# Kernel tuning notes

Hardware: AMD Instinct MI355X
Metric: run time of the kernel (lower is better)

Reference implementation:

```python
import jax, jax.numpy as jnp
import numpy as np

HEAD_DIM = 128
MAX_TIMESCALE = 10000.0
MIN_TIMESCALE = 1.0


def _rope(x, pos):
    # x: [B, S, H, D], pos: [B, S]
    d = x.shape[-1]
    fraction = 2.0 * jnp.arange(0, d // 2, dtype=jnp.float32) / d
    timescale = MIN_TIMESCALE * (MAX_TIMESCALE / MIN_TIMESCALE) ** fraction  # [D/2]
    sinusoid = pos.astype(jnp.float32)[..., None, None] / timescale  # [B,S,1,D/2]
    sin, cos = jnp.sin(sinusoid), jnp.cos(sinusoid)
    xf = x.astype(jnp.float32)
    x1, x2 = jnp.split(xf, 2, axis=-1)
    return jnp.concatenate((x1 * cos - x2 * sin, x2 * cos + x1 * sin), axis=-1).astype(x.dtype)


def setup_inputs() -> dict:
    key = jax.random.key(0)
    ks = jax.random.split(key, 5)
    B, T, D, N, K, H = 2, 2048, 2048, 16, 4, HEAD_DIM
    s = 0.02
    X = jax.random.normal(ks[0], (B, T, D), dtype=jnp.float32)
    q_positions = jnp.broadcast_to(jnp.arange(T, dtype=jnp.int32), (B, T))
    Wq = jax.random.normal(ks[1], (D, N, H), dtype=jnp.float32) * s
    Wk = jax.random.normal(ks[2], (D, K, H), dtype=jnp.float32) * s
    Wv = jax.random.normal(ks[3], (D, K, H), dtype=jnp.float32) * s
    Wo = jax.random.normal(ks[4], (N, H, D), dtype=jnp.float32) * s
    return {"X": X, "q_positions": q_positions, "Wq": Wq, "Wk": Wk, "Wv": Wv, "Wo": Wo}


def reference(X, q_positions, Wq, Wk, Wv, Wo):
    B, T, D = X.shape
    N, K = Wq.shape[1], Wk.shape[1]
    groups = N // K
    # fused QKV projections (DenseGeneral, no bias)
    q = jnp.einsum('btd,dnh->btnh', X, Wq)  # [B,T,N,H]
    k = jnp.einsum('btd,dkh->btkh', X, Wk)  # [B,T,K,H]
    v = jnp.einsum('btd,dkh->btkh', X, Wv)  # [B,T,K,H]
    # RoPE (note: original uses q_positions sin/cos for both q and k in the no-cache path)
    q = _rope(q, q_positions)
    k = _rope(k, q_positions)
    # GQA: broadcast kv heads to query heads
    k = jnp.repeat(k, groups, axis=2)  # [B,T,N,H]
    v = jnp.repeat(v, groups, axis=2)
    # attention with scale=1.0 and causal masking
    scores = jnp.einsum('btnh,bsnh->bnts', q, k)  # [B,N,T,T]
    causal = jnp.tril(jnp.ones((T, T), dtype=bool))
    scores = jnp.where(causal, scores, jnp.finfo(scores.dtype).min)
    probs = jax.nn.softmax(scores, axis=-1)
    attn = jnp.einsum('bnts,bsnh->btnh', probs, v)  # [B,T,N,H]
    # output projection contracting (head, head_dim)
    out = jnp.einsum('btnh,nhd->btd', attn, Wo)
    return out.astype(X.dtype)
```

## Files before the change

kernel.cpp:

```cpp
#include <hip/hip_runtime.h>
#include <math.h>

#define DEVI static __device__ __forceinline__

using f16x8 = __attribute__((ext_vector_type(8))) _Float16;
using h16x2 = __attribute__((ext_vector_type(2))) __fp16;
using f32x4  = __attribute__((ext_vector_type(4))) float;
using f32x16 = __attribute__((ext_vector_type(16))) float;

constexpr int Bb = 2, Tt = 2048, Dd = 2048, NQ = 16, NK = 4, HD = 128;
constexpr int Mrows = Bb * Tt;
constexpr int QKVC  = NQ*HD + 2*NK*HD;
constexpr int KOFF  = NQ*HD;
constexpr int VOFF  = NQ*HD + NK*HD;

DEVI ushort f2h(float f) {
  _Float16 h = (_Float16)f;
  union { _Float16 h; ushort u; } v; v.h = h;
  return v.u;
}
DEVI float h2f(ushort u) {
  union { ushort u; _Float16 h; } v; v.u = u;
  return (float)v.h;
}

typedef const __attribute__((address_space(1))) unsigned* gp1;
typedef __attribute__((address_space(3))) unsigned* lp3;
DEVI void gload16(void* lds, const void* g) {
  __builtin_amdgcn_global_load_lds((gp1)g, (lp3)lds, 16, 0, 0);
}

__global__ void k_cvt(const float* __restrict__ x, ushort* __restrict__ o, int n4) {
  int i = blockIdx.x * blockDim.x + threadIdx.x;
  if (i >= n4) return;
  float4 v = ((const float4*)x)[i];
  ushort4 u;
  u.x = f2h(v.x); u.y = f2h(v.y); u.z = f2h(v.z); u.w = f2h(v.w);
  ((ushort4*)o)[i] = u;
}

__global__ void k_tconv(const float* __restrict__ in, ushort* __restrict__ out, int R, int C) {
  __shared__ float t[32][33];
  const int c0 = blockIdx.x * 32, r0 = blockIdx.y * 32;
  const int tx = threadIdx.x, ty = threadIdx.y;
#pragma unroll
  for (int i = 0; i < 32; i += 8)
    t[ty + i][tx] = in[(size_t)(r0 + ty + i) * C + (c0 + tx)];
  __syncthreads();
#pragma unroll
  for (int i = 0; i < 32; i += 8)
    out[(size_t)(c0 + ty + i) * R + (r0 + tx)] = f2h(t[tx][ty + i]);
}

DEVI void stv(float* p, float v)  { *p = v; }
DEVI void stv(ushort* p, float v) { *p = f2h(v); }

template <typename OT>
__launch_bounds__(256)
__global__ void k_gemm_bt(const ushort* __restrict__ A, const ushort* __restrict__ Bt,
                          OT* __restrict__ C, int M, int N, int Kd) {
  __shared__ char As[8192];
  __shared__ char Bs[8192];
  const int tid = threadIdx.x;
  const int l = tid & 63, w = tid >> 6;
  const int wr = w >> 1, wc = w & 1;
  const int lr = l & 15, lk = l >> 4;
  const size_t row0 = (size_t)blockIdx.y * 128, col0 = (size_t)blockIdx.x * 128;

  f32x4 acc[4][4];
#pragma unroll
  for (int i = 0; i < 4; ++i)
#pragma unroll
    for (int j = 0; j < 4; ++j) acc[i][j] = (f32x4){0.f, 0.f, 0.f, 0.f};

  const int c0i = tid, c1i = tid + 256;
  const int ra0 = c0i >> 2, sa0 = (c0i & 3) ^ ((ra0 >> 1) & 3);
  const int ra1 = c1i >> 2, sa1 = (c1i & 3) ^ ((ra1 >> 1) & 3);

  for (int kt = 0; kt < Kd; kt += 32) {
    if (kt) __syncthreads();
    gload16(As + c0i * 16, A + (row0 + ra0) * Kd + kt + sa0 * 8);
    gload16(As + c1i * 16, A + (row0 + ra1) * Kd + kt + sa1 * 8);
    gload16(Bs + c0i * 16, Bt + (col0 + ra0) * Kd + kt + sa0 * 8);
    gload16(Bs + c1i * 16, Bt + (col0 + ra1) * Kd + kt + sa1 * 8);
    __syncthreads();
    f16x8 af[4], bfr[4];
#pragma unroll
    for (int i = 0; i < 4; ++i) {
      int ra = wr * 64 + i * 16 + lr;
      af[i] = *(const f16x8*)(As + ra * 64 + ((lk ^ ((ra >> 1) & 3)) << 4));
      int rb = wc * 64 + i * 16 + lr;
      bfr[i] = *(const f16x8*)(Bs + rb * 64 + ((lk ^ ((rb >> 1) & 3)) << 4));
    }
#pragma unroll
    for (int i = 0; i < 4; ++i)
#pragma unroll
      for (int j = 0; j < 4; ++j)
        acc[i][j] = __builtin_amdgcn_mfma_f32_16x16x32_f16(af[i], bfr[j], acc[i][j], 0, 0, 0);
  }
#pragma unroll
  for (int i = 0; i < 4; ++i) {
    size_t r = row0 + wr * 64 + i * 16 + lk * 4;
#pragma unroll
    for (int j = 0; j < 4; ++j) {
      size_t cc = col0 + wc * 64 + j * 16 + lr;
#pragma unroll
      for (int rg = 0; rg < 4; ++rg) stv(&C[(r + rg) * N + cc], acc[i][j][rg]);
    }
  }
}

__global__ void k_rope_tab(const int* __restrict__ pos, float* __restrict__ tab) {
  int idx = blockIdx.x * blockDim.x + threadIdx.x;
  if (idx >= Mrows * 64) return;
  int m = idx >> 6, i = idx & 63;
  double a = (double)pos[m] * exp2(-0.20762050593045952 * (double)i);
  tab[idx * 2]     = (float)cos(a);
  tab[idx * 2 + 1] = (float)sin(a);
}

__global__ void k_rope(ushort* __restrict__ qkv, const float* __restrict__ tab) {
  int idx = blockIdx.x * blockDim.x + threadIdx.x;
  if (idx >= Mrows * 20 * 8) return;
  int chunk = idx & 7;
  int h20 = (idx >> 3) % 20;
  int m = idx / 160;
  int colbase = (h20 < 16) ? h20 * 128 : (KOFF + (h20 - 16) * 128);
  size_t base = (size_t)m * QKVC + colbase + chunk * 8;
  union { uint4 v; ushort s[8]; } A1, A2, O1, O2;
  A1.v = *(const uint4*)(qkv + base);
  A2.v = *(const uint4*)(qkv + base + 64);
  const float* tp = tab + ((size_t)m * 64 + chunk * 8) * 2;
#pragma unroll
  for (int j = 0; j < 8; ++j) {
    float c = tp[2 * j], s = tp[2 * j + 1];
    float x1 = h2f(A1.s[j]), x2 = h2f(A2.s[j]);
    O1.s[j] = f2h(x1 * c - x2 * s);
    O2.s[j] = f2h(x2 * c + x1 * s);
  }
  *(uint4*)(qkv + base) = O1.v;
  *(uint4*)(qkv + base + 64) = O2.v;
}

__global__ void k_vt(const ushort* __restrict__ qkv, ushort* __restrict__ vt) {
  __shared__ ushort t[32][33];
  const int bg = blockIdx.z, bq = bg >> 2, g = bg & 3;
  const int s0 = blockIdx.x * 32, h0 = blockIdx.y * 32;
  const int tx = threadIdx.x, ty = threadIdx.y;
#pragma unroll
  for (int i = 0; i < 32; i += 8)
    t[ty + i][tx] = qkv[(size_t)(bq * Tt + s0 + ty + i) * QKVC + VOFF + g * HD + h0 + tx];
  __syncthreads();
  const int sx = (tx & 3) | ((tx & 8) >> 1) | ((tx & 4) << 1) | (tx & 16);
#pragma unroll
  for (int i = 0; i < 32; i += 8)
    vt[((size_t)bg * HD + h0 + ty + i) * Tt + (s0 + sx)] = t[tx][ty + i];
}

__launch_bounds__(256, 2)
__global__ void k_flash(const ushort* __restrict__ qkv, const ushort* __restrict__ vt,
                        ushort* __restrict__ attn) {
  __shared__ char Ks[2][16384];
  __shared__ char Vs[2][16384];
  const int b = blockIdx.x;
  const int vv = b >> 8, u = b & 255;
  const int hid = u >> 3, p = u & 7;
  const int qt = vv ? p : (15 - p);
  const int bq = hid >> 4, n = hid & 15, g = n >> 2;
  const int tid = threadIdx.x, w = tid >> 6, l = tid & 63;
  const int q5 = l & 31, hi = l >> 5;
  const int t0 = qt * 128;
  const int qrow = t0 + w * 32;
  const int qglob = qrow + q5;

  f16x8 qf[8];
  {
    const size_t qb = ((size_t)(bq * Tt + qglob)) * QKVC + n * HD + hi * 8;
#pragma unroll
    for (int kc = 0; kc < 8; ++kc) qf[kc] = *(const f16x8*)(qkv + qb + kc * 16);
  }
  f32x16 O[4];
#pragma unroll
  for (int ht = 0; ht < 4; ++ht)
#pragma unroll
    for (int r = 0; r < 16; ++r) O[ht][r] = 0.f;
  float m = -INFINITY, lsum = 0.f;

  const size_t kgbase = (size_t)(bq * Tt) * QKVC + KOFF + g * HD;
  const size_t vgbase = (size_t)(bq * 4 + g) * HD * Tt;
  const int ntiles = 2 * qt + 2;

#define STAGE(buf, s0s)                                                               \
  {                                                                                   \
    _Pragma("unroll")                                                                 \
    for (int cc = 0; cc < 4; ++cc) {                                                  \
      int c = cc * 256 + tid;                                                         \
      int sK = c >> 4, gK = (c & 15) ^ (sK & 15);                                     \
      gload16(Ks[buf] + c * 16, qkv + kgbase + (size_t)((s0s) + sK) * QKVC + gK * 8); \
      int hV = c >> 3, gV = (c & 7) ^ (hV & 7);                                       \
      gload16(Vs[buf] + c * 16, vt + vgbase + (size_t)hV * Tt + (s0s) + gV * 8);      \
    }                                                                                 \
  }

  STAGE(0, 0);
  __syncthreads();

  for (int j = 0; j < ntiles; ++j) {
    const int cur = j & 1;
    if (j + 1 < ntiles) STAGE(cur ^ 1, (j + 1) * 64);
    const int s0 = j * 64;
    if (s0 <= qrow + 31) {
      f32x16 sc[2];
      __builtin_amdgcn_s_setprio(1);
#pragma unroll
      for (int st = 0; st < 2; ++st) {
        f32x16 a;
#pragma unroll
        for (int r = 0; r < 16; ++r) a[r] = 0.f;
        const int sl = st * 32 + q5;
        const int ssw = (sl & 15) << 4;
#pragma unroll
        for (int kc = 0; kc < 8; ++kc) {
          f16x8 kf = *(const f16x8*)(Ks[cur] + sl * 256 + (((kc * 32 + hi * 16)) ^ ssw));
          a = __builtin_amdgcn_mfma_f32_32x32x16_f16(kf, qf[kc], a, 0, 0, 0);
        }
        sc[st] = a;
      }
      __builtin_amdgcn_s_setprio(0);
      if (s0 + 63 > qrow) {
#pragma unroll
        for (int st = 0; st < 2; ++st)
#pragma unroll
          for (int r = 0; r < 16; ++r) {
            int sg = s0 + st * 32 + (r & 3) + 8 * (r >> 2) + 4 * hi;
            if (sg > qglob) sc[st][r] = -INFINITY;
          }
      }
      float pm = -INFINITY;
#pragma unroll
      for (int st = 0; st < 2; ++st)
#pragma unroll
        for (int r = 0; r < 16; ++r) pm = fmaxf(pm, sc[st][r]);
      pm = fmaxf(pm, __shfl_xor(pm, 32));
      const bool doresc = !__all(pm - m <= 8.0f);
      float scl = 1.f;
      if (doresc) { float mn = fmaxf(m, pm); scl = __expf(m - mn); m = mn; }
      float rs = 0.f;
#pragma unroll
      for (int st = 0; st < 2; ++st)
#pragma unroll
        for (int r = 0; r < 16; ++r) { sc[st][r] = __expf(sc[st][r] - m); rs += sc[st][r]; }
      rs += __shfl_xor(rs, 32);
      if (doresc) {
        float sr[16];
#pragma unroll
        for (int r = 0; r < 16; ++r) sr[r] = __shfl(scl, (r & 3) + 8 * (r >> 2) + 4 * hi);
#pragma unroll
        for (int ht = 0; ht < 4; ++ht)
#pragma unroll
          for (int r = 0; r < 16; ++r) O[ht][r] *= sr[r];
        lsum = lsum * scl + rs;
      } else {
        lsum += rs;
      }
      unsigned pw[2][8];
#pragma unroll
      for (int st = 0; st < 2; ++st)
#pragma unroll
        for (int i = 0; i < 8; ++i) {
          union { h16x2 h; unsigned u; } t;
          t.h = __builtin_amdgcn_cvt_pkrtz(sc[st][2 * i], sc[st][2 * i + 1]);
          pw[st][i] = t.u;
        }
      __builtin_amdgcn_s_setprio(1);
#pragma unroll
      for (int ht = 0; ht < 4; ++ht) {
        const int hrow = ht * 32 + q5;
        const int hsw = (hrow & 7) << 4;
#pragma unroll
        for (int cc = 0; cc < 4; ++cc) {
          const int st = cc >> 1, ch = cc & 1;
          union { unsigned u[4]; f16x8 v; } pa;
          pa.u[0] = pw[st][ch * 4 + 0];
          pa.u[1] = pw[st][ch * 4 + 1];
          pa.u[2] = pw[st][ch * 4 + 2];
          pa.u[3] = pw[st][ch * 4 + 3];
          f16x8 vf = *(const f16x8*)(Vs[cur] + hrow * 128 + (((cc * 2 + hi) << 4) ^ hsw));
          O[ht] = __builtin_amdgcn_mfma_f32_32x32x16_f16(pa.v, vf, O[ht], 0, 0, 0);
        }
      }
      __builtin_amdgcn_s_setprio(0);
    }
    __syncthreads();
  }
#undef STAGE
  float iv[16];
#pragma unroll
  for (int r = 0; r < 16; ++r) iv[r] = 1.f / __shfl(lsum, (r & 3) + 8 * (r >> 2) + 4 * hi);
#pragma unroll
  for (int ht = 0; ht < 4; ++ht)
#pragma unroll
    for (int r = 0; r < 16; ++r) {
      size_t orow = (size_t)(bq * Tt + qrow + (r & 3) + 8 * (r >> 2) + 4 * hi);
      attn[orow * 2048 + n * HD + ht * 32 + q5] = f2h(O[ht][r] * iv[r]);
    }
}

extern "C" void kernel_launch(void* const* d_in, const int* in_sizes, int n_in,
                              void* d_out, int out_size, void* d_ws, size_t ws_size,
                              hipStream_t stream) {
  const float* X  = (const float*)d_in[0];
  const int*   qp = (const int*)d_in[1];
  const float* Wq = (const float*)d_in[2];
  const float* Wk = (const float*)d_in[3];
  const float* Wv = (const float*)d_in[4];
  const float* Wo = (const float*)d_in[5];
  float* out = (float*)d_out;
  char* ws = (char*)d_ws;

  ushort* Xf    = (ushort*)(ws + 0);
  ushort* WqkvT = (ushort*)(ws + 16777216);
  ushort* WoT   = (ushort*)(ws + 29360128);
  ushort* QKV   = (ushort*)(ws + 37748736);
  ushort* VT    = (ushort*)(ws + 62914560);
  ushort* attn  = (ushort*)(ws + 67108864);
  float*  tab   = (float*)(ws + 83886080);

  dim3 tb(32, 8);
  k_cvt<<<(Mrows * Dd / 4 + 255) / 256, 256, 0, stream>>>(X, Xf, Mrows * Dd / 4);
  k_tconv<<<dim3(64, 64), tb, 0, stream>>>(Wq, WqkvT, Dd, NQ * HD);
  k_tconv<<<dim3(16, 64), tb, 0, stream>>>(Wk, WqkvT + (size_t)KOFF * Dd, Dd, NK * HD);
  k_tconv<<<dim3(16, 64), tb, 0, stream>>>(Wv, WqkvT + (size_t)VOFF * Dd, Dd, NK * HD);
  k_tconv<<<dim3(64, 64), tb, 0, stream>>>(Wo, WoT, NQ * HD, Dd);
  k_gemm_bt<ushort><<<dim3(QKVC / 128, Mrows / 128), 256, 0, stream>>>(
      Xf, WqkvT, QKV, Mrows, QKVC, Dd);
  k_rope_tab<<<(Mrows * 64 + 255) / 256, 256, 0, stream>>>(qp, tab);
  k_rope<<<(Mrows * 160 + 255) / 256, 256, 0, stream>>>(QKV, tab);
  k_vt<<<dim3(Tt / 32, HD / 32, Bb * NK), tb, 0, stream>>>(QKV, VT);
  k_flash<<<dim3(512), 256, 0, stream>>>(QKV, VT, attn);
  k_gemm_bt<float><<<dim3(Dd / 128, Mrows / 128), 256, 0, stream>>>(
      attn, WoT, out, Mrows, Dd, Dd);
}
```

Baseline: 219.0 us.

## Software-pipeline PV MFMA of previous tile behind current softmax with triple-buffered V

Restructures the flash-attention loop so the P·V matrix multiply for tile j-1 is issued after the max/rescale factor for tile j is known but before its exponentials. That lets MFMA work overlap the exp/convert VALU work. V staging moves to a three-slot LDS ring so the previous tile's V stays resident while the next is loaded, with extra drain steps after the loop. The per-tile cross-half row-sum shuffle is also deferred to a single reduction at the end. The cost is more LDS per block (80KB), which may pressure occupancy, plus more complex control flow around the causal boundary.

Result: no change. 219.3 us (+0.1%).

```diff
diff --git a/kernel.cpp b/kernel.cpp
--- a/kernel.cpp
+++ b/kernel.cpp
@@ -161,13 +161,13 @@
 __global__ void k_flash(const ushort* __restrict__ qkv, const ushort* __restrict__ vt,
                         ushort* __restrict__ attn) {
   __shared__ char Ks[2][16384];
-  __shared__ char Vs[2][16384];
+  __shared__ char Vs[3][16384];
   const int b = blockIdx.x;
   const int vv = b >> 8, u = b & 255;
   const int hid = u >> 3, p = u & 7;
   const int qt = vv ? p : (15 - p);
   const int bq = hid >> 4, n = hid & 15, g = n >> 2;
-  const int tid = threadIdx.x, w = tid >> 6, l = tid & 63;
+  const int tid = threadIdx.x, l = tid & 63, w = tid >> 6;
   const int q5 = l & 31, hi = l >> 5;
   const int t0 = qt * 128;
   const int qrow = t0 + w * 32;
@@ -185,31 +185,54 @@
 #pragma unroll
     for (int r = 0; r < 16; ++r) O[ht][r] = 0.f;
   float m = -INFINITY, lsum = 0.f;
+  unsigned pw[2][8];
 
   const size_t kgbase = (size_t)(bq * Tt) * QKVC + KOFF + g * HD;
   const size_t vgbase = (size_t)(bq * 4 + g) * HD * Tt;
   const int ntiles = 2 * qt + 2;
-
-#define STAGE(buf, s0s)                                                               \
-  {                                                                                   \
-    _Pragma("unroll")                                                                 \
-    for (int cc = 0; cc < 4; ++cc) {                                                  \
-      int c = cc * 256 + tid;                                                         \
-      int sK = c >> 4, gK = (c & 15) ^ (sK & 15);                                     \
-      gload16(Ks[buf] + c * 16, qkv + kgbase + (size_t)((s0s) + sK) * QKVC + gK * 8); \
-      int hV = c >> 3, gV = (c & 7) ^ (hV & 7);                                       \
-      gload16(Vs[buf] + c * 16, vt + vgbase + (size_t)hV * Tt + (s0s) + gV * 8);      \
-    }                                                                                 \
-  }
-
-  STAGE(0, 0);
+  const int myjmax = (qrow + 31) >> 6;
+
+#define STAGE(kb, vslot, s0s)                                                          \
+  {                                                                                    \
+    _Pragma("unroll")                                                                  \
+    for (int cc = 0; cc < 4; ++cc) {                                                   \
+      int c = cc * 256 + tid;                                                          \
+      int sK = c >> 4, gK = (c & 15) ^ (sK & 15);                                      \
+      gload16(Ks[kb] + c * 16, qkv + kgbase + (size_t)((s0s) + sK) * QKVC + gK * 8);   \
+      int hV = c >> 3, gV = (c & 7) ^ (hV & 7);                                        \
+      gload16(Vs[vslot] + c * 16, vt + vgbase + (size_t)hV * Tt + (s0s) + gV * 8);     \
+    }                                                                                  \
+  }
+
+#define PVSTEP(vbase)                                                                  \
+  {                                                                                    \
+    __builtin_amdgcn_s_setprio(1);                                                     \
+    _Pragma("unroll")                                                                  \
+    for (int ht = 0; ht < 4; ++ht) {                                                   \
+      const int hrow = ht * 32 + q5;                                                   \
+      const int hsw = (hrow & 7) << 4;                                                 \
+      _Pragma("unroll")                                                                \
+      for (int cc = 0; cc < 4; ++cc) {                                                 \
+        union { unsigned uu[4]; f16x8 v; } pa;                                         \
+        pa.uu[0] = pw[cc >> 1][(cc & 1) * 4 + 0];                                      \
+        pa.uu[1] = pw[cc >> 1][(cc & 1) * 4 + 1];                                      \
+        pa.uu[2] = pw[cc >> 1][(cc & 1) * 4 + 2];                                      \
+        pa.uu[3] = pw[cc >> 1][(cc & 1) * 4 + 3];                                      \
+        f16x8 vf = *(const f16x8*)((vbase) + hrow * 128 + (((cc * 2 + hi) << 4) ^ hsw)); \
+        O[ht] = __builtin_amdgcn_mfma_f32_32x32x16_f16(pa.v, vf, O[ht], 0, 0, 0);      \
+      }                                                                                \
+    }                                                                                  \
+    __builtin_amdgcn_s_setprio(0);                                                     \
+  }
+
+  STAGE(0, 0, 0);
   __syncthreads();
 
   for (int j = 0; j < ntiles; ++j) {
-    const int cur = j & 1;
-    if (j + 1 < ntiles) STAGE(cur ^ 1, (j + 1) * 64);
+    const int kcur = j & 1;
+    if (j + 1 < ntiles) STAGE(kcur ^ 1, (j + 1) % 3, (j + 1) * 64);
     const int s0 = j * 64;
-    if (s0 <= qrow + 31) {
+    if (j <= myjmax) {
       f32x16 sc[2];
       __builtin_amdgcn_s_setprio(1);
 #pragma unroll
@@ -221,7 +244,7 @@
         const int ssw = (sl & 15) << 4;
 #pragma unroll
         for (int kc = 0; kc < 8; ++kc) {
-          f16x8 kf = *(const f16x8*)(Ks[cur] + sl * 256 + (((kc * 32 + hi * 16)) ^ ssw));
+          f16x8 kf = *(const f16x8*)(Ks[kcur] + sl * 256 + (((kc * 32 + hi * 16)) ^ ssw));
           a = __builtin_amdgcn_mfma_f32_32x32x16_f16(kf, qf[kc], a, 0, 0, 0);
         }
         sc[st] = a;
@@ -245,12 +268,12 @@
       const bool doresc = !__all(pm - m <= 8.0f);
       float scl = 1.f;
       if (doresc) { float mn = fmaxf(m, pm); scl = __expf(m - mn); m = mn; }
+      if (j > 0) PVSTEP(Vs[(j + 2) % 3]);
       float rs = 0.f;
 #pragma unroll
       for (int st = 0; st < 2; ++st)
 #pragma unroll
         for (int r = 0; r < 16; ++r) { sc[st][r] = __expf(sc[st][r] - m); rs += sc[st][r]; }
-      rs += __shfl_xor(rs, 32);
       if (doresc) {
         float sr[16];
 #pragma unroll
@@ -263,7 +286,6 @@
       } else {
         lsum += rs;
       }
-      unsigned pw[2][8];
 #pragma unroll
       for (int st = 0; st < 2; ++st)
 #pragma unroll
@@ -272,31 +294,18 @@
           t.h = __builtin_amdgcn_cvt_pkrtz(sc[st][2 * i], sc[st][2 * i + 1]);
           pw[st][i] = t.u;
         }
-      __builtin_amdgcn_s_setprio(1);
-#pragma unroll
-      for (int ht = 0; ht < 4; ++ht) {
-        const int hrow = ht * 32 + q5;
-        const int hsw = (hrow & 7) << 4;
-#pragma unroll
-        for (int cc = 0; cc < 4; ++cc) {
-          const int st = cc >> 1, ch = cc & 1;
-          union { unsigned u[4]; f16x8 v; } pa;
-          pa.u[0] = pw[st][ch * 4 + 0];
-          pa.u[1] = pw[st][ch * 4 + 1];
-          pa.u[2] = pw[st][ch * 4 + 2];
-          pa.u[3] = pw[st][ch * 4 + 3];
-          f16x8 vf = *(const f16x8*)(Vs[cur] + hrow * 128 + (((cc * 2 + hi) << 4) ^ hsw));
-          O[ht] = __builtin_amdgcn_mfma_f32_32x32x16_f16(pa.v, vf, O[ht], 0, 0, 0);
-        }
-      }
-      __builtin_amdgcn_s_setprio(0);
+    } else if (j == myjmax + 1) {
+      PVSTEP(Vs[(j + 2) % 3]);
     }
     __syncthreads();
   }
+  if (myjmax == ntiles - 1) PVSTEP(Vs[myjmax % 3]);
 #undef STAGE
+#undef PVSTEP
+  const float ltot = lsum + __shfl_xor(lsum, 32);
   float iv[16];
 #pragma unroll
-  for (int r = 0; r < 16; ++r) iv[r] = 1.f / __shfl(lsum, (r & 3) + 8 * (r >> 2) + 4 * hi);
+  for (int r = 0; r < 16; ++r) iv[r] = 1.f / __shfl(ltot, (r & 3) + 8 * (r >> 2) + 4 * hi);
 #pragma unroll
   for (int ht = 0; ht < 4; ++ht)
 #pragma unroll
```

## Restructure flash attention to 128-key tiles with split K/V staging and exp2 softmax

Applied to the files above, without the earlier changes.

The flash kernel now processes 128-key tiles with single-buffered K and V in LDS. The next K tile loads while softmax runs and the next V tile loads after PV, with explicit waitcnt and barriers replacing the double-buffered per-64-key scheme. Q is pre-scaled by log2(e) in the RoPE kernel so softmax can use exp2f. The rescale threshold becomes 11 in log2 units, and the lsum cross-half shuffle is deferred to the end. These changes aim to cut loop overhead, barriers and per-tile shuffles. The risks are less overlap from single buffering and exposure of load latency.

Measured after the change: 296.2 us. 35.2% more time.

```diff
diff --git a/kernel.cpp b/kernel.cpp
--- a/kernel.cpp
+++ b/kernel.cpp
@@ -125,6 +125,7 @@
   int chunk = idx & 7;
   int h20 = (idx >> 3) % 20;
   int m = idx / 160;
+  const float qs = (h20 < 16) ? 1.4426950408889634f : 1.0f;
   int colbase = (h20 < 16) ? h20 * 128 : (KOFF + (h20 - 16) * 128);
   size_t base = (size_t)m * QKVC + colbase + chunk * 8;
   union { uint4 v; ushort s[8]; } A1, A2, O1, O2;
@@ -135,8 +136,8 @@
   for (int j = 0; j < 8; ++j) {
     float c = tp[2 * j], s = tp[2 * j + 1];
     float x1 = h2f(A1.s[j]), x2 = h2f(A2.s[j]);
-    O1.s[j] = f2h(x1 * c - x2 * s);
-    O2.s[j] = f2h(x2 * c + x1 * s);
+    O1.s[j] = f2h((x1 * c - x2 * s) * qs);
+    O2.s[j] = f2h((x2 * c + x1 * s) * qs);
   }
   *(uint4*)(qkv + base) = O1.v;
   *(uint4*)(qkv + base + 64) = O2.v;
@@ -160,17 +161,16 @@
 __launch_bounds__(256, 2)
 __global__ void k_flash(const ushort* __restrict__ qkv, const ushort* __restrict__ vt,
                         ushort* __restrict__ attn) {
-  __shared__ char Ks[2][16384];
-  __shared__ char Vs[2][16384];
+  __shared__ char Ks[32768];
+  __shared__ char Vs[32768];
   const int b = blockIdx.x;
   const int vv = b >> 8, u = b & 255;
   const int hid = u >> 3, p = u & 7;
   const int qt = vv ? p : (15 - p);
   const int bq = hid >> 4, n = hid & 15, g = n >> 2;
-  const int tid = threadIdx.x, w = tid >> 6, l = tid & 63;
+  const int tid = threadIdx.x, l = tid & 63, w = tid >> 6;
   const int q5 = l & 31, hi = l >> 5;
-  const int t0 = qt * 128;
-  const int qrow = t0 + w * 32;
+  const int qrow = qt * 128 + w * 32;
   const int qglob = qrow + q5;
 
   f16x8 qf[8];
@@ -188,115 +188,129 @@
 
   const size_t kgbase = (size_t)(bq * Tt) * QKVC + KOFF + g * HD;
   const size_t vgbase = (size_t)(bq * 4 + g) * HD * Tt;
-  const int ntiles = 2 * qt + 2;
-
-#define STAGE(buf, s0s)                                                               \
+  const int ntiles = qt + 1;
+
+#define STAGE_K(s0s)                                                                  \
   {                                                                                   \
     _Pragma("unroll")                                                                 \
-    for (int cc = 0; cc < 4; ++cc) {                                                  \
+    for (int cc = 0; cc < 8; ++cc) {                                                  \
       int c = cc * 256 + tid;                                                         \
       int sK = c >> 4, gK = (c & 15) ^ (sK & 15);                                     \
-      gload16(Ks[buf] + c * 16, qkv + kgbase + (size_t)((s0s) + sK) * QKVC + gK * 8); \
-      int hV = c >> 3, gV = (c & 7) ^ (hV & 7);                                       \
-      gload16(Vs[buf] + c * 16, vt + vgbase + (size_t)hV * Tt + (s0s) + gV * 8);      \
+      gload16(Ks + c * 16, qkv + kgbase + (size_t)((s0s) + sK) * QKVC + gK * 8);      \
     }                                                                                 \
   }
-
-  STAGE(0, 0);
+#define STAGE_V(s0s)                                                                  \
+  {                                                                                   \
+    _Pragma("unroll")                                                                 \
+    for (int cc = 0; cc < 8; ++cc) {                                                  \
+      int c = cc * 256 + tid;                                                         \
+      int hV = c >> 4, gV = (c & 15) ^ (hV & 15);                                     \
+      gload16(Vs + c * 16, vt + vgbase + (size_t)hV * Tt + (s0s) + gV * 8);           \
+    }                                                                                 \
+  }
+
+  STAGE_K(0);
+  STAGE_V(0);
   __syncthreads();
 
   for (int j = 0; j < ntiles; ++j) {
-    const int cur = j & 1;
-    if (j + 1 < ntiles) STAGE(cur ^ 1, (j + 1) * 64);
-    const int s0 = j * 64;
-    if (s0 <= qrow + 31) {
-      f32x16 sc[2];
-      __builtin_amdgcn_s_setprio(1);
-#pragma unroll
-      for (int st = 0; st < 2; ++st) {
-        f32x16 a;
-#pragma unroll
-        for (int r = 0; r < 16; ++r) a[r] = 0.f;
-        const int sl = st * 32 + q5;
-        const int ssw = (sl & 15) << 4;
-#pragma unroll
-        for (int kc = 0; kc < 8; ++kc) {
-          f16x8 kf = *(const f16x8*)(Ks[cur] + sl * 256 + (((kc * 32 + hi * 16)) ^ ssw));
-          a = __builtin_amdgcn_mfma_f32_32x32x16_f16(kf, qf[kc], a, 0, 0, 0);
+    const int s0 = j * 128;
+    f32x16 sc[4];
+    __builtin_amdgcn_s_setprio(1);
+#pragma unroll
+    for (int st = 0; st < 4; ++st) {
+      f32x16 a;
+#pragma unroll
+      for (int r = 0; r < 16; ++r) a[r] = 0.f;
+      const int sl = st * 32 + q5;
+      const int ssw = (sl & 15) << 4;
+#pragma unroll
+      for (int kc = 0; kc < 8; ++kc) {
+        f16x8 kf = *(const f16x8*)(Ks + sl * 256 + ((kc * 32 + hi * 16) ^ ssw));
+        a = __builtin_amdgcn_mfma_f32_32x32x16_f16(kf, qf[kc], a, 0, 0, 0);
+      }
+      sc[st] = a;
+    }
+    __builtin_amdgcn_s_setprio(0);
+    __syncthreads();
+    if (j + 1 < ntiles) STAGE_K(s0 + 128);
+    if (j == ntiles - 1) {
+#pragma unroll
+      for (int st = 0; st < 4; ++st)
+#pragma unroll
+        for (int r = 0; r < 16; ++r) {
+          int sg = s0 + st * 32 + (r & 3) + 8 * (r >> 2) + 4 * hi;
+          if (sg > qglob) sc[st][r] = -INFINITY;
         }
-        sc[st] = a;
+    }
+    float pm = -INFINITY;
+#pragma unroll
+    for (int st = 0; st < 4; ++st)
+#pragma unroll
+      for (int r = 0; r < 16; ++r) pm = fmaxf(pm, sc[st][r]);
+    pm = fmaxf(pm, __shfl_xor(pm, 32));
+    const bool doresc = !__all(pm - m <= 11.0f);
+    float scl = 1.f;
+    if (doresc) { float mn = fmaxf(m, pm); scl = exp2f(m - mn); m = mn; }
+    float rs = 0.f;
+#pragma unroll
+    for (int st = 0; st < 4; ++st)
+#pragma unroll
+      for (int r = 0; r < 16; ++r) { sc[st][r] = exp2f(sc[st][r] - m); rs += sc[st][r]; }
+    if (doresc) {
+      float sr[16];
+#pragma unroll
+      for (int r = 0; r < 16; ++r) sr[r] = __shfl(scl, (r & 3) + 8 * (r >> 2) + 4 * hi);
+#pragma unroll
+      for (int ht = 0; ht < 4; ++ht)
+#pragma unroll
+        for (int r = 0; r < 16; ++r) O[ht][r] *= sr[r];
+      lsum = lsum * scl + rs;
+    } else {
+      lsum += rs;
+    }
+    unsigned pw[4][8];
+#pragma unroll
+    for (int st = 0; st < 4; ++st)
+#pragma unroll
+      for (int i = 0; i < 8; ++i) {
+        union { h16x2 h; unsigned u; } t;
+        t.h = __builtin_amdgcn_cvt_pkrtz(sc[st][2 * i], sc[st][2 * i + 1]);
+        pw[st][i] = t.u;
       }
-      __builtin_amdgcn_s_setprio(0);
-      if (s0 + 63 > qrow) {
-#pragma unroll
-        for (int st = 0; st < 2; ++st)
-#pragma unroll
-          for (int r = 0; r < 16; ++r) {
-            int sg = s0 + st * 32 + (r & 3) + 8 * (r >> 2) + 4 * hi;
-            if (sg > qglob) sc[st][r] = -INFINITY;
-          }
-      }
-      float pm = -INFINITY;
-#pragma unroll
-      for (int st = 0; st < 2; ++st)
-#pragma unroll
-        for (int r = 0; r < 16; ++r) pm = fmaxf(pm, sc[st][r]);
-      pm = fmaxf(pm, __shfl_xor(pm, 32));
-      const bool doresc = !__all(pm - m <= 8.0f);
-      float scl = 1.f;
-      if (doresc) { float mn = fmaxf(m, pm); scl = __expf(m - mn); m = mn; }
-      float rs = 0.f;
-#pragma unroll
-      for (int st = 0; st < 2; ++st)
-#pragma unroll
-        for (int r = 0; r < 16; ++r) { sc[st][r] = __expf(sc[st][r] - m); rs += sc[st][r]; }
-      rs += __shfl_xor(rs, 32);
-      if (doresc) {
-        float sr[16];
-#pragma unroll
-        for (int r = 0; r < 16; ++r) sr[r] = __shfl(scl, (r & 3) + 8 * (r >> 2) + 4 * hi);
-#pragma unroll
-        for (int ht = 0; ht < 4; ++ht)
-#pragma unroll
-          for (int r = 0; r < 16; ++r) O[ht][r] *= sr[r];
-        lsum = lsum * scl + rs;
-      } else {
-        lsum += rs;
-      }
-      unsigned pw[2][8];
-#pragma unroll
-      for (int st = 0; st < 2; ++st)
-#pragma unroll
-        for (int i = 0; i < 8; ++i) {
-          union { h16x2 h; unsigned u; } t;
-          t.h = __builtin_amdgcn_cvt_pkrtz(sc[st][2 * i], sc[st][2 * i + 1]);
-          pw[st][i] = t.u;
-        }
-      __builtin_amdgcn_s_setprio(1);
-#pragma unroll
-      for (int ht = 0; ht < 4; ++ht) {
-        const int hrow = ht * 32 + q5;
-        const int hsw = (hrow & 7) << 4;
-#pragma unroll
-        for (int cc = 0; cc < 4; ++cc) {
-          const int st = cc >> 1, ch = cc & 1;
-          union { unsigned u[4]; f16x8 v; } pa;
-          pa.u[0] = pw[st][ch * 4 + 0];
-          pa.u[1] = pw[st][ch * 4 + 1];
-          pa.u[2] = pw[st][ch * 4 + 2];
-          pa.u[3] = pw[st][ch * 4 + 3];
-          f16x8 vf = *(const f16x8*)(Vs[cur] + hrow * 128 + (((cc * 2 + hi) << 4) ^ hsw));
+    __builtin_amdgcn_s_setprio(1);
+#pragma unroll
+    for (int ht = 0; ht < 4; ++ht) {
+      const int hrow = ht * 32 + q5;
+      const int hsw = (hrow & 15) << 4;
+#pragma unroll
+      for (int st = 0; st < 4; ++st)
+#pragma unroll
+        for (int ch = 0; ch < 2; ++ch) {
+          union { unsigned uu[4]; f16x8 v; } pa;
+          pa.uu[0] = pw[st][ch * 4 + 0];
+          pa.uu[1] = pw[st][ch * 4 + 1];
+          pa.uu[2] = pw[st][ch * 4 + 2];
+          pa.uu[3] = pw[st][ch * 4 + 3];
+          f16x8 vf = *(const f16x8*)(Vs + hrow * 256 + ((st * 64 + ch * 32 + hi * 16) ^ hsw));
           O[ht] = __builtin_amdgcn_mfma_f32_32x32x16_f16(pa.v, vf, O[ht], 0, 0, 0);
         }
-      }
-      __builtin_amdgcn_s_setprio(0);
-    }
-    __syncthreads();
-  }
-#undef STAGE
+    }
+    __builtin_amdgcn_s_setprio(0);
+    __builtin_amdgcn_s_barrier();
+    if (j + 1 < ntiles) {
+      STAGE_V(s0 + 128);
+      asm volatile("s_waitcnt vmcnt(8)" ::: "memory");
+    }
+    __builtin_amdgcn_s_barrier();
+    __builtin_amdgcn_sched_barrier(0);
+  }
+#undef STAGE_K
+#undef STAGE_V
+  const float ltot = lsum + __shfl_xor(lsum, 32);
   float iv[16];
 #pragma unroll
-  for (int r = 0; r < 16; ++r) iv[r] = 1.f / __shfl(lsum, (r & 3) + 8 * (r >> 2) + 4 * hi);
+  for (int r = 0; r < 16; ++r) iv[r] = 1.f / __shfl(ltot, (r & 3) + 8 * (r >> 2) + 4 * hi);
 #pragma unroll
   for (int ht = 0; ht < 4; ++ht)
 #pragma unroll
```

## Split long causal query tiles across two blocks and merge partials; use exp2 softmax

Applied to the files above, without the earlier changes.

The eight largest query tiles per head are each split into two KV ranges handled by separate blocks, which write normalized partial outputs plus (max, sum) to workspace. A new merge kernel combines the two halves, and the smaller tiles run unsplit. The aim is better load balance across the 768 blocks, at the cost of an extra launch and extra global traffic. Q is also pre-scaled by log2(e) in the RoPE kernel so softmax can use exp2f, and the lazy-rescale threshold is raised, which shifts how partial sums are kept in fp16.

Result: slower. 240.4 us (+9.7%).

```diff
diff --git a/kernel.cpp b/kernel.cpp
--- a/kernel.cpp
+++ b/kernel.cpp
@@ -125,6 +125,7 @@
   int chunk = idx & 7;
   int h20 = (idx >> 3) % 20;
   int m = idx / 160;
+  const float qs = (h20 < 16) ? 1.4426950408889634f : 1.0f;
   int colbase = (h20 < 16) ? h20 * 128 : (KOFF + (h20 - 16) * 128);
   size_t base = (size_t)m * QKVC + colbase + chunk * 8;
   union { uint4 v; ushort s[8]; } A1, A2, O1, O2;
@@ -135,8 +136,8 @@
   for (int j = 0; j < 8; ++j) {
     float c = tp[2 * j], s = tp[2 * j + 1];
     float x1 = h2f(A1.s[j]), x2 = h2f(A2.s[j]);
-    O1.s[j] = f2h(x1 * c - x2 * s);
-    O2.s[j] = f2h(x2 * c + x1 * s);
+    O1.s[j] = f2h((x1 * c - x2 * s) * qs);
+    O2.s[j] = f2h((x2 * c + x1 * s) * qs);
   }
   *(uint4*)(qkv + base) = O1.v;
   *(uint4*)(qkv + base + 64) = O2.v;
@@ -159,18 +160,33 @@
 
 __launch_bounds__(256, 2)
 __global__ void k_flash(const ushort* __restrict__ qkv, const ushort* __restrict__ vt,
-                        ushort* __restrict__ attn) {
+                        ushort* __restrict__ attn, ushort* __restrict__ pOn,
+                        float2* __restrict__ pml) {
   __shared__ char Ks[2][16384];
   __shared__ char Vs[2][16384];
   const int b = blockIdx.x;
-  const int vv = b >> 8, u = b & 255;
-  const int hid = u >> 3, p = u & 7;
-  const int qt = vv ? p : (15 - p);
+  int qt, hid, j0, j1, sp = 0, half = 0;
+  bool split;
+  if (b < 512) {
+    split = true;
+    half = b & 1;
+    sp = b >> 1;
+    qt = 15 - (b >> 6);
+    hid = sp & 31;
+    j0 = half ? (qt + 1) : 0;
+    j1 = half ? (2 * qt + 2) : (qt + 1);
+  } else {
+    split = false;
+    int c = b - 512;
+    qt = 7 - (c >> 5);
+    hid = c & 31;
+    j0 = 0;
+    j1 = 2 * qt + 2;
+  }
   const int bq = hid >> 4, n = hid & 15, g = n >> 2;
-  const int tid = threadIdx.x, w = tid >> 6, l = tid & 63;
+  const int tid = threadIdx.x, l = tid & 63, w = tid >> 6;
   const int q5 = l & 31, hi = l >> 5;
-  const int t0 = qt * 128;
-  const int qrow = t0 + w * 32;
+  const int qrow = qt * 128 + w * 32;
   const int qglob = qrow + q5;
 
   f16x8 qf[8];
@@ -188,7 +204,6 @@
 
   const size_t kgbase = (size_t)(bq * Tt) * QKVC + KOFF + g * HD;
   const size_t vgbase = (size_t)(bq * 4 + g) * HD * Tt;
-  const int ntiles = 2 * qt + 2;
 
 #define STAGE(buf, s0s)                                                               \
   {                                                                                   \
@@ -202,12 +217,12 @@
     }                                                                                 \
   }
 
-  STAGE(0, 0);
+  STAGE(0, j0 * 64);
   __syncthreads();
 
-  for (int j = 0; j < ntiles; ++j) {
-    const int cur = j & 1;
-    if (j + 1 < ntiles) STAGE(cur ^ 1, (j + 1) * 64);
+  for (int j = j0; j < j1; ++j) {
+    const int cur = (j - j0) & 1;
+    if (j + 1 < j1) STAGE(cur ^ 1, (j + 1) * 64);
     const int s0 = j * 64;
     if (s0 <= qrow + 31) {
       f32x16 sc[2];
@@ -242,15 +257,14 @@
 #pragma unroll
         for (int r = 0; r < 16; ++r) pm = fmaxf(pm, sc[st][r]);
       pm = fmaxf(pm, __shfl_xor(pm, 32));
-      const bool doresc = !__all(pm - m <= 8.0f);
+      const bool doresc = !__all(pm - m <= 11.0f);
       float scl = 1.f;
-      if (doresc) { float mn = fmaxf(m, pm); scl = __expf(m - mn); m = mn; }
+      if (doresc) { float mn = fmaxf(m, pm); scl = exp2f(m - mn); m = mn; }
       float rs = 0.f;
 #pragma unroll
       for (int st = 0; st < 2; ++st)
 #pragma unroll
-        for (int r = 0; r < 16; ++r) { sc[st][r] = __expf(sc[st][r] - m); rs += sc[st][r]; }
-      rs += __shfl_xor(rs, 32);
+        for (int r = 0; r < 16; ++r) { sc[st][r] = exp2f(sc[st][r] - m); rs += sc[st][r]; }
       if (doresc) {
         float sr[16];
 #pragma unroll
@@ -279,12 +293,11 @@
         const int hsw = (hrow & 7) << 4;
 #pragma unroll
         for (int cc = 0; cc < 4; ++cc) {
-          const int st = cc >> 1, ch = cc & 1;
-          union { unsigned u[4]; f16x8 v; } pa;
-          pa.u[0] = pw[st][ch * 4 + 0];
-          pa.u[1] = pw[st][ch * 4 + 1];
-          pa.u[2] = pw[st][ch * 4 + 2];
-          pa.u[3] = pw[st][ch * 4 + 3];
+          union { unsigned uu[4]; f16x8 v; } pa;
+          pa.uu[0] = pw[cc >> 1][(cc & 1) * 4 + 0];
+          pa.uu[1] = pw[cc >> 1][(cc & 1) * 4 + 1];
+          pa.uu[2] = pw[cc >> 1][(cc & 1) * 4 + 2];
+          pa.uu[3] = pw[cc >> 1][(cc & 1) * 4 + 3];
           f16x8 vf = *(const f16x8*)(Vs[cur] + hrow * 128 + (((cc * 2 + hi) << 4) ^ hsw));
           O[ht] = __builtin_amdgcn_mfma_f32_32x32x16_f16(pa.v, vf, O[ht], 0, 0, 0);
         }
@@ -294,16 +307,60 @@
     __syncthreads();
   }
 #undef STAGE
+  const float ltot = lsum + __shfl_xor(lsum, 32);
   float iv[16];
 #pragma unroll
-  for (int r = 0; r < 16; ++r) iv[r] = 1.f / __shfl(lsum, (r & 3) + 8 * (r >> 2) + 4 * hi);
-#pragma unroll
-  for (int ht = 0; ht < 4; ++ht)
-#pragma unroll
-    for (int r = 0; r < 16; ++r) {
-      size_t orow = (size_t)(bq * Tt + qrow + (r & 3) + 8 * (r >> 2) + 4 * hi);
-      attn[orow * 2048 + n * HD + ht * 32 + q5] = f2h(O[ht][r] * iv[r]);
+  for (int r = 0; r < 16; ++r) iv[r] = 1.f / __shfl(ltot, (r & 3) + 8 * (r >> 2) + 4 * hi);
+  if (!split) {
+#pragma unroll
+    for (int ht = 0; ht < 4; ++ht)
+#pragma unroll
+      for (int r = 0; r < 16; ++r) {
+        size_t orow = (size_t)(bq * Tt + qrow + (r & 3) + 8 * (r >> 2) + 4 * hi);
+        attn[orow * 2048 + n * HD + ht * 32 + q5] = f2h(O[ht][r] * iv[r]);
+      }
+  } else {
+    ushort* po = pOn + ((size_t)(sp * 2 + half)) * (128 * 128);
+#pragma unroll
+    for (int ht = 0; ht < 4; ++ht)
+#pragma unroll
+      for (int r = 0; r < 16; ++r) {
+        int rl = w * 32 + (r & 3) + 8 * (r >> 2) + 4 * hi;
+        po[rl * 128 + ht * 32 + q5] = f2h(O[ht][r] * iv[r]);
+      }
+    if (hi == 0) pml[(sp * 2 + half) * 128 + w * 32 + q5] = make_float2(m, ltot);
+  }
+}
+
+__global__ void k_merge(const ushort* __restrict__ pOn, const float2* __restrict__ pml,
+                        ushort* __restrict__ attn) {
+  const int sp = blockIdx.x;
+  const int qt = 15 - (sp >> 5), hid = sp & 31;
+  const int bq = hid >> 4, n = hid & 15;
+  const int t = threadIdx.x;
+  const int row = t >> 1, cpart = (t & 1) * 64;
+  float2 ml0 = pml[(sp * 2 + 0) * 128 + row];
+  float2 ml1 = pml[(sp * 2 + 1) * 128 + row];
+  float mm = fmaxf(ml0.x, ml1.x);
+  float w0 = ml0.y * exp2f(ml0.x - mm);
+  float w1 = ml1.y * exp2f(ml1.x - mm);
+  float inv = 1.f / (w0 + w1);
+  w0 *= inv; w1 *= inv;
+  const ushort* p0 = pOn + ((size_t)(sp * 2 + 0)) * 16384 + row * 128 + cpart;
+  const ushort* p1 = pOn + ((size_t)(sp * 2 + 1)) * 16384 + row * 128 + cpart;
+  size_t orow = (size_t)(bq * Tt + qt * 128 + row);
+  ushort* ao = attn + orow * 2048 + n * HD + cpart;
+#pragma unroll
+  for (int i = 0; i < 64; i += 8) {
+    uint4 a = *(const uint4*)(p0 + i), bv = *(const uint4*)(p1 + i);
+    ushort o[8];
+#pragma unroll
+    for (int k2 = 0; k2 < 8; ++k2) {
+      float f0 = h2f(((const ushort*)&a)[k2]), f1 = h2f(((const ushort*)&bv)[k2]);
+      o[k2] = f2h(f0 * w0 + f1 * w1);
     }
+    *(uint4*)(ao + i) = *(uint4*)o;
+  }
 }
 
 extern "C" void kernel_launch(void* const* d_in, const int* in_sizes, int n_in,
@@ -325,6 +382,8 @@
   ushort* VT    = (ushort*)(ws + 62914560);
   ushort* attn  = (ushort*)(ws + 67108864);
   float*  tab   = (float*)(ws + 83886080);
+  ushort* pOn   = (ushort*)(ws + 85983232);
+  float2* pml   = (float2*)(ws + 102760448);
 
   dim3 tb(32, 8);
   k_cvt<<<(Mrows * Dd / 4 + 255) / 256, 256, 0, stream>>>(X, Xf, Mrows * Dd / 4);
@@ -337,7 +396,8 @@
   k_rope_tab<<<(Mrows * 64 + 255) / 256, 256, 0, stream>>>(qp, tab);
   k_rope<<<(Mrows * 160 + 255) / 256, 256, 0, stream>>>(QKV, tab);
   k_vt<<<dim3(Tt / 32, HD / 32, Bb * NK), tb, 0, stream>>>(QKV, VT);
-  k_flash<<<dim3(512), 256, 0, stream>>>(QKV, VT, attn);
+  k_flash<<<dim3(768), 256, 0, stream>>>(QKV, VT, attn, pOn, pml);
+  k_merge<<<dim3(256), 256, 0, stream>>>(pOn, pml, attn);
   k_gemm_bt<float><<<dim3(Dd / 128, Mrows / 128), 256, 0, stream>>>(
       attn, WoT, out, Mrows, Dd, Dd);
 }
```
